# Optimization experiments

Measured on AMD Instinct MI355X. Metric: run time of the kernel, lower is better.

## Reference

```python
import jax, jax.numpy as jnp
import numpy as np

H = 16      # n_heads
HD = 48     # head_dim
D = H * HD  # d_model = 768
DZ = 128    # pair dim
EPS = 1e-5


def setup_inputs() -> dict:
    key = jax.random.key(0)
    ks = jax.random.split(key, 12)
    B, S = 1, 1024
    sc = 0.02
    return {
        "s": jax.random.normal(ks[0], (B, S, D), jnp.float32),
        "z": jax.random.normal(ks[1], (B, S, S, DZ), jnp.float32),
        "Wq": jax.random.normal(ks[2], (D, D), jnp.float32) * sc,
        "bq": jax.random.normal(ks[3], (D,), jnp.float32) * sc,
        "Wk": jax.random.normal(ks[4], (D, D), jnp.float32) * sc,
        "Wv": jax.random.normal(ks[5], (D, D), jnp.float32) * sc,
        "Wg": jax.random.normal(ks[6], (D, D), jnp.float32) * sc,
        "ln_w": jnp.ones((DZ,), jnp.float32),
        "ln_b": jnp.zeros((DZ,), jnp.float32),
        "Wz": jax.random.normal(ks[7], (H, DZ), jnp.float32) * sc,
        "Wo": jax.random.normal(ks[8], (D, D), jnp.float32) * sc,
    }


def reference(s, z, Wq, bq, Wk, Wv, Wg, ln_w, ln_b, Wz, Wo):
    B, S, _ = s.shape
    # fused QKV projection (q has bias; k, v do not)
    q = (s @ Wq.T + bq).reshape(B, S, H, HD).transpose(0, 2, 1, 3)  # [B,H,S,hd]
    k = (s @ Wk.T).reshape(B, S, H, HD).transpose(0, 2, 1, 3)
    v = (s @ Wv.T).reshape(B, S, H, HD).transpose(0, 2, 1, 3)
    # pair bias: LayerNorm(z) then Linear(DZ -> H), used as additive attn bias
    mu = jnp.mean(z, axis=-1, keepdims=True)
    var = jnp.mean(jnp.square(z - mu), axis=-1, keepdims=True)
    zn = (z - mu) * jax.lax.rsqrt(var + EPS) * ln_w + ln_b
    bias = jnp.einsum('bstc,hc->bhst', zn, Wz)  # [B,H,S,S]
    # scaled dot-product attention with pair bias
    scores = jnp.einsum('bhsd,bhtd->bhst', q, k) * (HD ** -0.5) + bias
    a = jax.nn.softmax(scores, axis=-1)
    o = jnp.einsum('bhst,bhtd->bhsd', a, v)           # [B,H,S,hd]
    o = o.transpose(0, 2, 1, 3).reshape(B, S, D)      # [B,S,D]
    # sigmoid gating and output projection
    g = s @ Wg.T
    o = o * jax.nn.sigmoid(g)
    return o @ Wo.T
```

## Files before the change

kernel.cpp:

```cpp
#include <hip/hip_runtime.h>

constexpr int H  = 16;
constexpr int HD = 48;
constexpr int D  = 768;
constexpr int DZ = 128;
constexpr int S  = 1024;
constexpr float EPS = 1e-5f;

typedef __attribute__((ext_vector_type(8))) short bf16x8;
typedef __attribute__((ext_vector_type(4))) float f32x4;

__device__ __forceinline__ float sigmoidf_(float x) { return 1.f / (1.f + __expf(-x)); }

__device__ __forceinline__ unsigned short f2b(float f) {
  unsigned u = __float_as_uint(f);
  u += 0x7FFFu + ((u >> 16) & 1u);
  return (unsigned short)(u >> 16);
}
__device__ __forceinline__ void split2(float x, unsigned short& h, unsigned short& l) {
  const unsigned short hb = f2b(x);
  const float hf = __uint_as_float((unsigned)hb << 16);
  h = hb;
  l = f2b(x - hf);
}
__device__ __forceinline__ unsigned pack2(unsigned short a, unsigned short b) {
  return (unsigned)a | ((unsigned)b << 16);
}

__global__ __launch_bounds__(256)
void prep_kernel(const float* __restrict__ s, const float* __restrict__ Wq,
                 const float* __restrict__ Wk, const float* __restrict__ Wv,
                 const float* __restrict__ Wg, const float* __restrict__ Wo,
                 unsigned short* __restrict__ s_hi,
                 unsigned short* __restrict__ w_hi, unsigned short* __restrict__ w_lo,
                 const float* __restrict__ Wz, const float* __restrict__ ln_w,
                 const float* __restrict__ ln_b, unsigned short* __restrict__ wzwb,
                 float* __restrict__ s12,
                 unsigned short* __restrict__ q_hi, unsigned short* __restrict__ k_hi) {
  if (blockIdx.x >= 769) {
    const int pid = (blockIdx.x - 769) * 6 + blockIdx.y;
    if (pid < 256) {
      const int i = pid * 256 + threadIdx.x;
      const int row = i >> 6, rem = i & 63;
      const int h = rem >> 2, off = (rem & 3) << 2;
      const size_t a = (size_t)row * 1024 + h * 64 + 48 + off;
      const ushort4 zz = {0, 0, 0, 0};
      *reinterpret_cast<ushort4*>(q_hi + a) = zz;
      *reinterpret_cast<ushort4*>(k_hi + a) = zz;
    }
    return;
  }
  if (blockIdx.x == 768) {
    if (blockIdx.y != 0) return;
    const int t = threadIdx.x;
    for (int e = t; e < 16 * DZ; e += 256) wzwb[e] = f2b(Wz[e] * ln_w[e & 127]);
    __syncthreads();
    if (t < 32) {
      const int h = t & 15;
      float a = 0.f;
      if (t < 16) {
        for (int c = 0; c < DZ; ++c) {
          const unsigned u = (unsigned)wzwb[h * DZ + c] << 16;
          a += __uint_as_float(u);
        }
      } else {
        for (int c = 0; c < DZ; ++c) a += Wz[h * DZ + c] * ln_b[c];
      }
      s12[t] = a;
    }
    return;
  }
  const int seg = blockIdx.y;
  const float* src;
  unsigned short* dh;
  unsigned short* dl = nullptr;
  int n;
  if (seg == 0) { src = s; dh = s_hi; n = S * D; }
  else {
    src = (seg == 1) ? Wq : (seg == 2) ? Wk : (seg == 3) ? Wv : (seg == 4) ? Wg : Wo;
    dh = w_hi + (size_t)(seg - 1) * D * D;
    if (seg == 5) dl = w_lo;
    n = D * D;
  }
  const int i4 = blockIdx.x * 256 + threadIdx.x;
  if (i4 * 4 < n) {
    const float4 v = *reinterpret_cast<const float4*>(src + (size_t)i4 * 4);
    ushort4 hh, ll;
    split2(v.x, hh.x, ll.x); split2(v.y, hh.y, ll.y);
    split2(v.z, hh.z, ll.z); split2(v.w, hh.w, ll.w);
    *reinterpret_cast<ushort4*>(dh + (size_t)i4 * 4) = hh;
    if (dl) *reinterpret_cast<ushort4*>(dl + (size_t)i4 * 4) = ll;
  }
}

__device__ __forceinline__ void mfma_core32_bf(const unsigned short* __restrict__ Ah,
                                               const unsigned short* __restrict__ Wh,
                                               const int m0, const int n0,
                                               const int k0, const int k1,
                                               f32x4& a00, f32x4& a01, f32x4& a10, f32x4& a11) {
  const int lane = threadIdx.x & 63;
  const int r16 = lane & 15, kg = lane >> 4;
  const unsigned short* pah = Ah + (size_t)(m0 + r16) * D + kg * 8;
  const unsigned short* pbh = Wh + (size_t)(n0 + r16) * D + kg * 8;
#pragma unroll 2
  for (int k = k0; k < k1; k += 32) {
    const bf16x8 ah0 = *reinterpret_cast<const bf16x8*>(pah + k);
    const bf16x8 ah1 = *reinterpret_cast<const bf16x8*>(pah + 16 * D + k);
    const bf16x8 bh0 = *reinterpret_cast<const bf16x8*>(pbh + k);
    const bf16x8 bh1 = *reinterpret_cast<const bf16x8*>(pbh + 16 * D + k);
    a00 = __builtin_amdgcn_mfma_f32_16x16x32_bf16(ah0, bh0, a00, 0, 0, 0);
    a01 = __builtin_amdgcn_mfma_f32_16x16x32_bf16(ah0, bh1, a01, 0, 0, 0);
    a10 = __builtin_amdgcn_mfma_f32_16x16x32_bf16(ah1, bh0, a10, 0, 0, 0);
    a11 = __builtin_amdgcn_mfma_f32_16x16x32_bf16(ah1, bh1, a11, 0, 0, 0);
  }
}

__global__ __launch_bounds__(256)
void qkvg_mfma_kernel(const unsigned short* __restrict__ s_hi,
                      const unsigned short* __restrict__ w_hi,
                      const float* __restrict__ bq,
                      unsigned short* __restrict__ q_hi,
                      unsigned short* __restrict__ k_hi,
                      unsigned short* __restrict__ vt_hi,
                      float* __restrict__ g_ws) {
  __shared__ float TT[4][32 * 33];
  __shared__ float CB[2][64][17];
  const int wv = threadIdx.x >> 6;
  const int pair = wv >> 1;
  const int khalf = wv & 1;
  const int tileid = blockIdx.x * 2 + pair;
  const int wsel = tileid / 768;
  const int rr = tileid % 768;
  const int m0 = (rr / 24) * 32, n0 = (rr % 24) * 32;
  f32x4 a00 = {0.f, 0.f, 0.f, 0.f}, a01 = a00, a10 = a00, a11 = a00;
  mfma_core32_bf(s_hi, w_hi + (size_t)wsel * D * D,
                 m0, n0, khalf * 384, khalf * 384 + 384, a00, a01, a10, a11);
  const int lane = threadIdx.x & 63;
  const int r16 = lane & 15, kg = lane >> 4;
  const float scale = 0.14433756729740643f;

  if (khalf == 1) {
#pragma unroll
    for (int r = 0; r < 4; ++r) {
      CB[pair][lane][r] = a00[r];
      CB[pair][lane][4 + r] = a01[r];
      CB[pair][lane][8 + r] = a10[r];
      CB[pair][lane][12 + r] = a11[r];
    }
  }
  __syncthreads();
  if (khalf == 1) return;
#pragma unroll
  for (int r = 0; r < 4; ++r) {
    a00[r] += CB[pair][lane][r];
    a01[r] += CB[pair][lane][4 + r];
    a10[r] += CB[pair][lane][8 + r];
    a11[r] += CB[pair][lane][12 + r];
  }

  float* T = TT[wv];
#pragma unroll
  for (int r = 0; r < 4; ++r) {
    T[(kg * 4 + r) * 33 + r16] = a00[r];
    T[(kg * 4 + r) * 33 + 16 + r16] = a01[r];
    T[(16 + kg * 4 + r) * 33 + r16] = a10[r];
    T[(16 + kg * 4 + r) * 33 + 16 + r16] = a11[r];
  }
  const int rr2 = lane >> 1, run = lane & 1;
  if (wsel <= 1) {
    const int row = m0 + rr2;
    const int col0 = n0 + run * 16;
    const int hcol0 = (col0 / 48) * 64 + (col0 % 48);
    unsigned short* dh = (wsel == 0) ? q_hi : k_hi;
#pragma unroll
    for (int p4 = 0; p4 < 4; ++p4) {
      float v0 = T[rr2 * 33 + run * 16 + p4 * 4 + 0];
      float v1 = T[rr2 * 33 + run * 16 + p4 * 4 + 1];
      float v2 = T[rr2 * 33 + run * 16 + p4 * 4 + 2];
      float v3 = T[rr2 * 33 + run * 16 + p4 * 4 + 3];
      if (wsel == 0) {
        v0 = (v0 + bq[col0 + p4 * 4 + 0]) * scale;
        v1 = (v1 + bq[col0 + p4 * 4 + 1]) * scale;
        v2 = (v2 + bq[col0 + p4 * 4 + 2]) * scale;
        v3 = (v3 + bq[col0 + p4 * 4 + 3]) * scale;
      }
      uint2 uh;
      uh.x = pack2(f2b(v0), f2b(v1)); uh.y = pack2(f2b(v2), f2b(v3));
      *reinterpret_cast<uint2*>(dh + (size_t)row * 1024 + hcol0 + p4 * 4) = uh;
    }
  } else if (wsel == 2) {
    const int c = lane >> 1;
    const int run2 = lane & 1;
    const int vc = n0 + c;
#pragma unroll
    for (int p4 = 0; p4 < 4; ++p4) {
      uint2 uh;
      uh.x = pack2(f2b(T[(run2 * 16 + p4 * 4 + 0) * 33 + c]),
                   f2b(T[(run2 * 16 + p4 * 4 + 1) * 33 + c]));
      uh.y = pack2(f2b(T[(run2 * 16 + p4 * 4 + 2) * 33 + c]),
                   f2b(T[(run2 * 16 + p4 * 4 + 3) * 33 + c]));
      *reinterpret_cast<uint2*>(vt_hi + (size_t)vc * 1024 + m0 + run2 * 16 + p4 * 4) = uh;
    }
  } else {
    const int row = m0 + rr2;
#pragma unroll
    for (int p4 = 0; p4 < 4; ++p4) {
      float4 v4;
      v4.x = T[rr2 * 33 + run * 16 + p4 * 4 + 0];
      v4.y = T[rr2 * 33 + run * 16 + p4 * 4 + 1];
      v4.z = T[rr2 * 33 + run * 16 + p4 * 4 + 2];
      v4.w = T[rr2 * 33 + run * 16 + p4 * 4 + 3];
      *reinterpret_cast<float4*>(g_ws + (size_t)row * D + n0 + run * 16 + p4 * 4) = v4;
    }
  }
}

__global__ __launch_bounds__(256)
void pair_bias_kernel(const float* __restrict__ z, const unsigned short* __restrict__ wzwb,
                      const float* __restrict__ s12, float* __restrict__ bias_out) {
  __shared__ float T[4][64 * 17];
  const int tid = threadIdx.x;
  const int lane = tid & 63;
  const int wv = tid >> 6;
  const int hq = lane & 15;
  const int grp = lane >> 4;

  bf16x8 bf[4];
#pragma unroll
  for (int m = 0; m < 4; ++m)
    bf[m] = *reinterpret_cast<const bf16x8*>(wzwb + hq * DZ + m * 32 + grp * 8);
  const float S1h = s12[hq], S2h = s12[16 + hq];

  const int chunk = blockIdx.x * 4 + wv;
  const size_t p0 = (size_t)chunk * 64;
  float* Tw = &T[wv][0];

#pragma unroll 1
  for (int sub = 0; sub < 4; ++sub) {
    const float* zr = z + (p0 + sub * 16 + hq) * DZ + grp * 8;
    f32x4 acc = {0.f, 0.f, 0.f, 0.f};
    float s1 = 0.f, s2 = 0.f;
#pragma unroll
    for (int m = 0; m < 4; ++m) {
      const float4 a0 = *reinterpret_cast<const float4*>(zr + m * 32);
      const float4 a1 = *reinterpret_cast<const float4*>(zr + m * 32 + 4);
      s1 += (a0.x + a0.y) + (a0.z + a0.w) + (a1.x + a1.y) + (a1.z + a1.w);
      s2 = fmaf(a0.x, a0.x, fmaf(a0.y, a0.y, fmaf(a0.z, a0.z, fmaf(a0.w, a0.w, s2))));
      s2 = fmaf(a1.x, a1.x, fmaf(a1.y, a1.y, fmaf(a1.z, a1.z, fmaf(a1.w, a1.w, s2))));
      bf16x8 af;
      af[0] = (short)f2b(a0.x); af[1] = (short)f2b(a0.y);
      af[2] = (short)f2b(a0.z); af[3] = (short)f2b(a0.w);
      af[4] = (short)f2b(a1.x); af[5] = (short)f2b(a1.y);
      af[6] = (short)f2b(a1.z); af[7] = (short)f2b(a1.w);
      acc = __builtin_amdgcn_mfma_f32_16x16x32_bf16(af, bf[m], acc, 0, 0, 0);
    }
    s1 += __shfl_xor(s1, 16); s1 += __shfl_xor(s1, 32);
    s2 += __shfl_xor(s2, 16); s2 += __shfl_xor(s2, 32);
    const float mu = s1 * (1.f / DZ);
    const float inv = rsqrtf(s2 * (1.f / DZ) - mu * mu + EPS);
#pragma unroll
    for (int r = 0; r < 4; ++r) {
      const int st = grp * 4 + r;
      const float mur = __shfl(mu, st);
      const float invr = __shfl(inv, st);
      Tw[(sub * 16 + st) * 17 + hq] = invr * (acc[r] - mur * S1h) + S2h;
    }
  }
#pragma unroll
  for (int hh = 0; hh < 16; ++hh)
    bias_out[(size_t)hh * S * S + p0 + lane] = Tw[lane * 17 + hh];
}

constexpr int PST = 72;
constexpr int PRS = 52;

__global__ __launch_bounds__(256)
void attn_kernel(const unsigned short* __restrict__ q_hi,
                 const unsigned short* __restrict__ k_hi,
                 const unsigned short* __restrict__ vt_hi,
                 const float* __restrict__ bias, const float* __restrict__ g,
                 unsigned short* __restrict__ a_hi) {
  __shared__ unsigned short Ph[4][16 * PST], Pl[4][16 * PST];
  __shared__ float Pr[4][16 * PRS];
  const int lane = threadIdx.x & 63;
  const int wv = threadIdx.x >> 6;
  const int h = blockIdx.x >> 6;
  const int qb = blockIdx.x & 63;
  const int q0 = qb << 4;
  const int n16 = lane & 15, kg = lane >> 4;

  const size_t qbase = (size_t)(q0 + n16) * 1024 + h * 64;
  const bf16x8 qh0 = *reinterpret_cast<const bf16x8*>(q_hi + qbase + kg * 8);
  const bf16x8 qh1 = *reinterpret_cast<const bf16x8*>(q_hi + qbase + 32 + kg * 8);

  float mrow = -1e30f, lrow = 0.f;
  f32x4 accO[3] = {};
  unsigned short* php = Ph[wv];
  unsigned short* plp = Pl[wv];

#pragma unroll 1
  for (int t0 = wv * 256; t0 < wv * 256 + 256; t0 += 64) {
    f32x4 sc[4];
#pragma unroll
    for (int ts = 0; ts < 4; ++ts) {
      const size_t kb = (size_t)(t0 + ts * 16 + n16) * 1024 + h * 64;
      const bf16x8 kh0 = *reinterpret_cast<const bf16x8*>(k_hi + kb + kg * 8);
      const bf16x8 kh1 = *reinterpret_cast<const bf16x8*>(k_hi + kb + 32 + kg * 8);
      f32x4 a = *reinterpret_cast<const f32x4*>(
          bias + ((size_t)h * S + (q0 + n16)) * S + t0 + ts * 16 + kg * 4);
      a = __builtin_amdgcn_mfma_f32_16x16x32_bf16(kh0, qh0, a, 0, 0, 0);
      a = __builtin_amdgcn_mfma_f32_16x16x32_bf16(kh1, qh1, a, 0, 0, 0);
      sc[ts] = a;
    }

    float tmax = sc[0][0];
#pragma unroll
    for (int ts = 0; ts < 4; ++ts)
#pragma unroll
      for (int r = 0; r < 4; ++r) tmax = fmaxf(tmax, sc[ts][r]);
    tmax = fmaxf(tmax, __shfl_xor(tmax, 16));
    tmax = fmaxf(tmax, __shfl_xor(tmax, 32));
    const float mn = fmaxf(mrow, tmax);
    const float fac = __expf(mrow - mn);
    mrow = mn;
    float psum = 0.f;
#pragma unroll
    for (int ts = 0; ts < 4; ++ts) {
      const float p0_ = __expf(sc[ts][0] - mn), p1_ = __expf(sc[ts][1] - mn);
      const float p2_ = __expf(sc[ts][2] - mn), p3_ = __expf(sc[ts][3] - mn);
      psum += (p0_ + p1_) + (p2_ + p3_);
      unsigned short h0, l0, h1, l1, h2, l2, h3, l3;
      split2(p0_, h0, l0); split2(p1_, h1, l1); split2(p2_, h2, l2); split2(p3_, h3, l3);
      const int ti = ts * 16 + kg * 4;
      unsigned* wh = reinterpret_cast<unsigned*>(&php[n16 * PST + ti]);
      unsigned* wl = reinterpret_cast<unsigned*>(&plp[n16 * PST + ti]);
      wh[0] = pack2(h0, h1); wh[1] = pack2(h2, h3);
      wl[0] = pack2(l0, l1); wl[1] = pack2(l2, l3);
    }
    lrow = lrow * fac + psum;

    float facr[4];
#pragma unroll
    for (int r = 0; r < 4; ++r) facr[r] = __shfl(fac, kg * 4 + r);
#pragma unroll
    for (int ds = 0; ds < 3; ++ds)
#pragma unroll
      for (int r = 0; r < 4; ++r) accO[ds][r] *= facr[r];

#pragma unroll
    for (int c = 0; c < 2; ++c) {
      const bf16x8 pah = *reinterpret_cast<const bf16x8*>(&php[n16 * PST + c * 32 + kg * 8]);
      const bf16x8 pal = *reinterpret_cast<const bf16x8*>(&plp[n16 * PST + c * 32 + kg * 8]);
#pragma unroll
      for (int ds = 0; ds < 3; ++ds) {
        const size_t vb = (size_t)(h * 48 + ds * 16 + n16) * 1024 + t0 + c * 32 + kg * 8;
        const bf16x8 vh = *reinterpret_cast<const bf16x8*>(vt_hi + vb);
        accO[ds] = __builtin_amdgcn_mfma_f32_16x16x32_bf16(pah, vh, accO[ds], 0, 0, 0);
        accO[ds] = __builtin_amdgcn_mfma_f32_16x16x32_bf16(pal, vh, accO[ds], 0, 0, 0);
      }
    }
  }

  lrow += __shfl_xor(lrow, 16);
  lrow += __shfl_xor(lrow, 32);

  float* pw = Pr[wv];
#pragma unroll
  for (int ds = 0; ds < 3; ++ds)
#pragma unroll
    for (int r = 0; r < 4; ++r)
      pw[(kg * 4 + r) * PRS + ds * 16 + n16] = accO[ds][r];
  if (kg == 0) {
    pw[n16 * PRS + 48] = mrow;
    pw[n16 * PRS + 49] = lrow;
  }
  __syncthreads();

  const int row = threadIdx.x >> 4;
  const int dsub = threadIdx.x & 15;
  const float m0_ = Pr[0][row * PRS + 48], m1_ = Pr[1][row * PRS + 48];
  const float m2_ = Pr[2][row * PRS + 48], m3_ = Pr[3][row * PRS + 48];
  const float l0_ = Pr[0][row * PRS + 49], l1_ = Pr[1][row * PRS + 49];
  const float l2_ = Pr[2][row * PRS + 49], l3_ = Pr[3][row * PRS + 49];
  const float M = fmaxf(fmaxf(m0_, m1_), fmaxf(m2_, m3_));
  const float e0 = __expf(m0_ - M), e1 = __expf(m1_ - M);
  const float e2 = __expf(m2_ - M), e3 = __expf(m3_ - M);
  const float rl = 1.f / (l0_ * e0 + l1_ * e1 + l2_ * e2 + l3_ * e3);
#pragma unroll
  for (int j = 0; j < 3; ++j) {
    const int d = dsub * 3 + j;
    const float o = (Pr[0][row * PRS + d] * e0 + Pr[1][row * PRS + d] * e1 +
                     Pr[2][row * PRS + d] * e2 + Pr[3][row * PRS + d] * e3) * rl;
    const size_t idx = (size_t)(q0 + row) * D + h * 48 + d;
    const float a = o * sigmoidf_(g[idx]);
    a_hi[idx] = f2b(a);
  }
}

__global__ __launch_bounds__(256)
void outproj_mfma_kernel(const unsigned short* __restrict__ a_hi,
                         const unsigned short* __restrict__ wo_hi,
                         const unsigned short* __restrict__ wo_lo,
                         float* __restrict__ out) {
  __shared__ float CB[2][64][9];
  const int wv = threadIdx.x >> 6;
  const int pair = wv >> 1;
  const int khalf = wv & 1;
  const int tileid = blockIdx.x * 2 + pair;
  const int m0 = (tileid / 48) * 32, n0 = (tileid % 48) * 16;
  const int lane = threadIdx.x & 63;
  const int r16 = lane & 15, kg = lane >> 4;
  const unsigned short* pah = a_hi + (size_t)(m0 + r16) * D + kg * 8;
  const unsigned short* pbh = wo_hi + (size_t)(n0 + r16) * D + kg * 8;
  const unsigned short* pbl = wo_lo + (size_t)(n0 + r16) * D + kg * 8;
  f32x4 a0 = {0.f, 0.f, 0.f, 0.f}, a1 = a0;
#pragma unroll 2
  for (int k = khalf * 384; k < khalf * 384 + 384; k += 32) {
    const bf16x8 ah0 = *reinterpret_cast<const bf16x8*>(pah + k);
    const bf16x8 ah1 = *reinterpret_cast<const bf16x8*>(pah + 16 * D + k);
    const bf16x8 bh0 = *reinterpret_cast<const bf16x8*>(pbh + k);
    const bf16x8 bl0 = *reinterpret_cast<const bf16x8*>(pbl + k);
    a0 = __builtin_amdgcn_mfma_f32_16x16x32_bf16(ah0, bh0, a0, 0, 0, 0);
    a0 = __builtin_amdgcn_mfma_f32_16x16x32_bf16(ah0, bl0, a0, 0, 0, 0);
    a1 = __builtin_amdgcn_mfma_f32_16x16x32_bf16(ah1, bh0, a1, 0, 0, 0);
    a1 = __builtin_amdgcn_mfma_f32_16x16x32_bf16(ah1, bl0, a1, 0, 0, 0);
  }
  if (khalf == 1) {
#pragma unroll
    for (int r = 0; r < 4; ++r) {
      CB[pair][lane][r] = a0[r];
      CB[pair][lane][4 + r] = a1[r];
    }
  }
  __syncthreads();
  if (khalf == 1) return;
#pragma unroll
  for (int r = 0; r < 4; ++r) {
    a0[r] += CB[pair][lane][r];
    a1[r] += CB[pair][lane][4 + r];
  }
#pragma unroll
  for (int r = 0; r < 4; ++r) {
    out[(size_t)(m0 + kg * 4 + r) * D + n0 + r16] = a0[r];
    out[(size_t)(m0 + 16 + kg * 4 + r) * D + n0 + r16] = a1[r];
  }
}

extern "C" void kernel_launch(void* const* d_in, const int* in_sizes, int n_in,
                              void* d_out, int out_size, void* d_ws, size_t ws_size,
                              hipStream_t stream) {
  const float* s    = (const float*)d_in[0];
  const float* z    = (const float*)d_in[1];
  const float* Wq   = (const float*)d_in[2];
  const float* bq   = (const float*)d_in[3];
  const float* Wk   = (const float*)d_in[4];
  const float* Wv   = (const float*)d_in[5];
  const float* Wg   = (const float*)d_in[6];
  const float* ln_w = (const float*)d_in[7];
  const float* ln_b = (const float*)d_in[8];
  const float* Wz   = (const float*)d_in[9];
  const float* Wo   = (const float*)d_in[10];
  float* out = (float*)d_out;

  float* g_ws    = (float*)d_ws;
  float* bias_ws = g_ws + (size_t)S * D;
  unsigned short* wzwb_ws = (unsigned short*)(bias_ws + (size_t)H * S * S);
  float* s12_ws  = bias_ws + (size_t)H * S * S + 1024;
  unsigned short* s_hi = (unsigned short*)(s12_ws + 32);
  unsigned short* w_hi = s_hi + (size_t)S * D;
  unsigned short* wo_lo = w_hi + (size_t)5 * D * D;
  unsigned short* a_hi = wo_lo + (size_t)D * D;
  unsigned short* q_hi = a_hi + (size_t)S * D;
  unsigned short* k_hi = q_hi + (size_t)S * 1024;
  unsigned short* vt_hi = k_hi + (size_t)S * 1024;

  prep_kernel<<<dim3(812, 6), 256, 0, stream>>>(s, Wq, Wk, Wv, Wg, Wo,
                                                s_hi, w_hi, wo_lo,
                                                Wz, ln_w, ln_b, wzwb_ws, s12_ws,
                                                q_hi, k_hi);
  qkvg_mfma_kernel<<<1536, 256, 0, stream>>>(s_hi, w_hi, bq,
                                             q_hi, k_hi, vt_hi, g_ws);
  pair_bias_kernel<<<4096, 256, 0, stream>>>(z, wzwb_ws, s12_ws, bias_ws);
  attn_kernel<<<1024, 256, 0, stream>>>(q_hi, k_hi, vt_hi,
                                        bias_ws, g_ws, a_hi);
  outproj_mfma_kernel<<<768, 256, 0, stream>>>(a_hi, w_hi + (size_t)4 * D * D,
                                               wo_lo, out);
}
```

Measured before the change: 236.4 us.

## Store pair bias in bf16 and drop low-part split of softmax probabilities

The pair-bias intermediate is now written as bf16 instead of fp32, which halves the 64 MB bias write and read traffic between the pair-bias and attention kernels. The attention kernel also drops the hi/lo bf16 split of the probabilities. That removes half of the P·V MFMAs, the low-part shared-memory buffer and the split arithmetic. The cost is lower accuracy in both the bias values and the probability weights, which may push results closer to the tolerance limit.

Measured after the change: 221.8 us, median of 2. -6.2%, faster.

```diff
diff --git a/kernel.cpp b/kernel.cpp
--- a/kernel.cpp
+++ b/kernel.cpp
@@ -16,6 +16,9 @@
   unsigned u = __float_as_uint(f);
   u += 0x7FFFu + ((u >> 16) & 1u);
   return (unsigned short)(u >> 16);
+}
+__device__ __forceinline__ float b2f(unsigned short u) {
+  return __uint_as_float((unsigned)u << 16);
 }
 __device__ __forceinline__ void split2(float x, unsigned short& h, unsigned short& l) {
   const unsigned short hb = f2b(x);
@@ -217,7 +220,7 @@
 
 __global__ __launch_bounds__(256)
 void pair_bias_kernel(const float* __restrict__ z, const unsigned short* __restrict__ wzwb,
-                      const float* __restrict__ s12, float* __restrict__ bias_out) {
+                      const float* __restrict__ s12, unsigned short* __restrict__ bias_out) {
   __shared__ float T[4][64 * 17];
   const int tid = threadIdx.x;
   const int lane = tid & 63;
@@ -268,7 +271,7 @@
   }
 #pragma unroll
   for (int hh = 0; hh < 16; ++hh)
-    bias_out[(size_t)hh * S * S + p0 + lane] = Tw[lane * 17 + hh];
+    bias_out[(size_t)hh * S * S + p0 + lane] = f2b(Tw[lane * 17 + hh]);
 }
 
 constexpr int PST = 72;
@@ -278,9 +281,9 @@
 void attn_kernel(const unsigned short* __restrict__ q_hi,
                  const unsigned short* __restrict__ k_hi,
                  const unsigned short* __restrict__ vt_hi,
-                 const float* __restrict__ bias, const float* __restrict__ g,
+                 const unsigned short* __restrict__ bias, const float* __restrict__ g,
                  unsigned short* __restrict__ a_hi) {
-  __shared__ unsigned short Ph[4][16 * PST], Pl[4][16 * PST];
+  __shared__ unsigned short Ph[4][16 * PST];
   __shared__ float Pr[4][16 * PRS];
   const int lane = threadIdx.x & 63;
   const int wv = threadIdx.x >> 6;
@@ -296,7 +299,6 @@
   float mrow = -1e30f, lrow = 0.f;
   f32x4 accO[3] = {};
   unsigned short* php = Ph[wv];
-  unsigned short* plp = Pl[wv];
 
 #pragma unroll 1
   for (int t0 = wv * 256; t0 < wv * 256 + 256; t0 += 64) {
@@ -306,8 +308,10 @@
       const size_t kb = (size_t)(t0 + ts * 16 + n16) * 1024 + h * 64;
       const bf16x8 kh0 = *reinterpret_cast<const bf16x8*>(k_hi + kb + kg * 8);
       const bf16x8 kh1 = *reinterpret_cast<const bf16x8*>(k_hi + kb + 32 + kg * 8);
-      f32x4 a = *reinterpret_cast<const f32x4*>(
-          bias + ((size_t)h * S + (q0 + n16)) * S + t0 + ts * 16 + kg * 4);
+      const ushort4 b4 = *reinterpret_cast<const ushort4*>(
+          bias + (size_t)h * S * S + (size_t)(q0 + n16) * S + t0 + ts * 16 + kg * 4);
+      f32x4 a;
+      a[0] = b2f(b4.x); a[1] = b2f(b4.y); a[2] = b2f(b4.z); a[3] = b2f(b4.w);
       a = __builtin_amdgcn_mfma_f32_16x16x32_bf16(kh0, qh0, a, 0, 0, 0);
       a = __builtin_amdgcn_mfma_f32_16x16x32_bf16(kh1, qh1, a, 0, 0, 0);
       sc[ts] = a;
@@ -329,13 +333,10 @@
       const float p0_ = __expf(sc[ts][0] - mn), p1_ = __expf(sc[ts][1] - mn);
       const float p2_ = __expf(sc[ts][2] - mn), p3_ = __expf(sc[ts][3] - mn);
       psum += (p0_ + p1_) + (p2_ + p3_);
-      unsigned short h0, l0, h1, l1, h2, l2, h3, l3;
-      split2(p0_, h0, l0); split2(p1_, h1, l1); split2(p2_, h2, l2); split2(p3_, h3, l3);
       const int ti = ts * 16 + kg * 4;
       unsigned* wh = reinterpret_cast<unsigned*>(&php[n16 * PST + ti]);
-      unsigned* wl = reinterpret_cast<unsigned*>(&plp[n16 * PST + ti]);
-      wh[0] = pack2(h0, h1); wh[1] = pack2(h2, h3);
-      wl[0] = pack2(l0, l1); wl[1] = pack2(l2, l3);
+      wh[0] = pack2(f2b(p0_), f2b(p1_));
+      wh[1] = pack2(f2b(p2_), f2b(p3_));
     }
     lrow = lrow * fac + psum;
 
@@ -350,13 +351,11 @@
 #pragma unroll
     for (int c = 0; c < 2; ++c) {
       const bf16x8 pah = *reinterpret_cast<const bf16x8*>(&php[n16 * PST + c * 32 + kg * 8]);
-      const bf16x8 pal = *reinterpret_cast<const bf16x8*>(&plp[n16 * PST + c * 32 + kg * 8]);
 #pragma unroll
       for (int ds = 0; ds < 3; ++ds) {
         const size_t vb = (size_t)(h * 48 + ds * 16 + n16) * 1024 + t0 + c * 32 + kg * 8;
         const bf16x8 vh = *reinterpret_cast<const bf16x8*>(vt_hi + vb);
         accO[ds] = __builtin_amdgcn_mfma_f32_16x16x32_bf16(pah, vh, accO[ds], 0, 0, 0);
-        accO[ds] = __builtin_amdgcn_mfma_f32_16x16x32_bf16(pal, vh, accO[ds], 0, 0, 0);
       }
     }
   }
@@ -463,10 +462,10 @@
   float* out = (float*)d_out;
 
   float* g_ws    = (float*)d_ws;
-  float* bias_ws = g_ws + (size_t)S * D;
-  unsigned short* wzwb_ws = (unsigned short*)(bias_ws + (size_t)H * S * S);
-  float* s12_ws  = bias_ws + (size_t)H * S * S + 1024;
-  unsigned short* s_hi = (unsigned short*)(s12_ws + 32);
+  float* s12_ws  = g_ws + (size_t)S * D;
+  unsigned short* bias16 = (unsigned short*)(s12_ws + 32);
+  unsigned short* wzwb_ws = bias16 + (size_t)H * S * S;
+  unsigned short* s_hi = wzwb_ws + 2048;
   unsigned short* w_hi = s_hi + (size_t)S * D;
   unsigned short* wo_lo = w_hi + (size_t)5 * D * D;
   unsigned short* a_hi = wo_lo + (size_t)D * D;
@@ -480,9 +479,9 @@
                                                 q_hi, k_hi);
   qkvg_mfma_kernel<<<1536, 256, 0, stream>>>(s_hi, w_hi, bq,
                                              q_hi, k_hi, vt_hi, g_ws);
-  pair_bias_kernel<<<4096, 256, 0, stream>>>(z, wzwb_ws, s12_ws, bias_ws);
+  pair_bias_kernel<<<4096, 256, 0, stream>>>(z, wzwb_ws, s12_ws, bias16);
   attn_kernel<<<1024, 256, 0, stream>>>(q_hi, k_hi, vt_hi,
-                                        bias_ws, g_ws, a_hi);
+                                        bias16, g_ws, a_hi);
   outproj_mfma_kernel<<<768, 256, 0, stream>>>(a_hi, w_hi + (size_t)4 * D * D,
                                                wo_lo, out);
 }
```
